# Kernel tuning notes

Measured on AMD Instinct MI355X. Metric: run time of the kernel, lower is better.

The kernel has to match this reference:

```python
import math
import jax, jax.numpy as jnp
import numpy as np

DIM = 128
NUM_PROJ = 256
ENC = jnp.asarray(2 ** np.arange(8), dtype=jnp.uint8)  # [1,2,4,...,128]
DEQUANT_SCALE = math.sqrt(math.pi / 2) / NUM_PROJ


def quantize_packed(x, S):
    # x: (..., dim) float32 -> packed uint8 (..., ceil(num_proj/8))
    projected = jnp.einsum('...d,pd->...p', x, S)
    signs = projected > 0  # bool (..., num_proj)
    pad_len = (-NUM_PROJ) % 8
    if pad_len > 0:
        pad = [(0, 0)] * (signs.ndim - 1) + [(0, pad_len)]
        signs = jnp.pad(signs, pad, constant_values=False)
    signs = signs.reshape(*signs.shape[:-1], -1, 8)  # (..., nbytes, 8)
    packed = jnp.sum(signs.astype(jnp.uint8) * ENC, axis=-1, dtype=jnp.uint8)
    return packed


def unpack_signs(packed):
    # packed: uint8 (..., nbytes) -> {-1,+1} float32 (..., num_proj)
    bits = jnp.bitwise_and(packed[..., None], ENC) > 0  # (..., nbytes, 8)
    bits = bits.reshape(*packed.shape[:-1], -1)[..., :NUM_PROJ]
    return bits.astype(jnp.float32) * 2.0 - 1.0


def setup_inputs() -> dict:
    key = jax.random.key(0)
    k1, k2, k3 = jax.random.split(key, 3)
    query = jax.random.normal(k1, (2, 32, 4096, DIM), dtype=jnp.float32)
    key_t = jax.random.normal(k2, (2, 32, 4096, DIM), dtype=jnp.float32)
    S = jax.random.normal(k3, (NUM_PROJ, DIM), dtype=jnp.float32)
    return {"query": query, "key": key_t, "S": S}


def reference(query, key, S):
    # quantize keys to bit-packed sign sketch, then estimate <query, key>
    packed = quantize_packed(key, S)                       # uint8 (..., 32)
    signs = unpack_signs(packed)                           # (..., 256)
    q_proj = jnp.einsum('...d,pd->...p', query, S)         # (..., 256)
    est = DEQUANT_SCALE * jnp.sum(q_proj * signs, axis=-1) # (B,H,S)
    return est
```

## Files before the change

kernel.cpp:

```cpp
#include <hip/hip_runtime.h>
#include <stdint.h>

#define DIM 128
#define NPROJ 256
#define TPB 128
#define TAU 0.016f
#define QCAP 512
#define DEQ 0.004895758348888673f

typedef _Float16 f16x8 __attribute__((ext_vector_type(8)));
typedef float f32x4 __attribute__((ext_vector_type(4)));

__global__ __launch_bounds__(256) void qjl_prep(const float* __restrict__ Sg,
                                                _Float16* __restrict__ ws) {
    int t = blockIdx.x * 256 + threadIdx.x;
    int lane = t & 63, fid = t >> 6;
    int f = fid & 1, ks = (fid >> 1) & 3, c = fid >> 3;
    int p = c * 32 + f * 16 + (lane & 15);
    int d0 = ks * 32 + (lane >> 4) * 8;
    const float4* s4 = (const float4*)(Sg + p * DIM + d0);
    float4 a = s4[0], b = s4[1];
    f16x8 h = {(_Float16)a.x, (_Float16)a.y, (_Float16)a.z, (_Float16)a.w,
               (_Float16)b.x, (_Float16)b.y, (_Float16)b.z, (_Float16)b.w};
    *(f16x8*)(ws + (size_t)fid * 512 + lane * 8) = h;
}

#define LOADT(buf, C, T)                                                             \
    { _Pragma("unroll")                                                              \
      for (int ks = 0; ks < 4; ++ks)                                                 \
          buf[ks] = *(const f16x8*)(bs + ((C) * 8 + ks * 2 + (T)) * 512 + lane * 8); }

#define LOADA(dst, src)                                                              \
    { const float* rp = (src) + (tok0 + wv * 16 + m) * DIM;                          \
      _Pragma("unroll")                                                              \
      for (int ks = 0; ks < 4; ++ks) {                                               \
          int d0 = ks * 32 + quad * 8;                                               \
          float4 x = *(const float4*)(rp + d0);                                      \
          float4 y = *(const float4*)(rp + d0 + 4);                                  \
          dst[ks] = (f16x8){(_Float16)x.x, (_Float16)x.y, (_Float16)x.z, (_Float16)x.w, \
                            (_Float16)y.x, (_Float16)y.y, (_Float16)y.z, (_Float16)y.w}; } }

#define F_STEP(C, T, buf)                                                            \
    { f32x4 k0 = {0,0,0,0}, q0 = {0,0,0,0};                                          \
      _Pragma("unroll")                                                              \
      for (int ks = 0; ks < 4; ++ks) {                                               \
          k0 = __builtin_amdgcn_mfma_f32_16x16x32_f16(ak[ks], buf[ks], k0, 0,0,0);   \
          q0 = __builtin_amdgcn_mfma_f32_16x16x32_f16(aq[ks], buf[ks], q0, 0,0,0);   \
      }                                                                              \
      _Pragma("unroll")                                                              \
      for (int r = 0; r < 4; ++r) {                                                  \
          uint32_t s0 = __float_as_uint(k0[r]) & 0x80000000u;                        \
          est[r] += __uint_as_float(__float_as_uint(q0[r]) ^ s0);                    \
          if (__builtin_expect(fabsf(k0[r]) < TAU, 0)) {                             \
              int idx = atomicAdd(&qn, 1);                                           \
              if (idx < QCAP) {                                                      \
                  qmeta[idx] = (uint32_t)(wv * 16 + quad * 4 + r)                    \
                      | ((uint32_t)((C) * 32 + (T) * 16 + m) << 8)                   \
                      | ((s0 ? 0u : 1u) << 16);                                      \
                  qval[idx] = q0[r];                                                 \
              }                                                                      \
          } } }

__global__ __launch_bounds__(512, 2) void qjl_main(
    const float* __restrict__ qg, const float* __restrict__ kg,
    const float* __restrict__ Sg, const _Float16* __restrict__ ws,
    float* __restrict__ out)
{
    __shared__ _Float16 bs[32768];
    __shared__ float    est_s[TPB];
    __shared__ uint32_t qmeta[QCAP];
    __shared__ float    qval[QCAP];
    __shared__ int      qn;

    const int tid = threadIdx.x, lane = tid & 63, wv = tid >> 6;
    const int m = lane & 15, quad = lane >> 4;
    const long tok0 = (long)blockIdx.x * TPB;
    if (tid == 0) qn = 0;

    {
        const char* gsrc = (const char*)ws + tid * 16;
        char* ldst = (char*)bs + tid * 16;
        #pragma unroll
        for (int r = 0; r < 8; ++r)
            __builtin_amdgcn_global_load_lds(
                (const __attribute__((address_space(1))) void*)(gsrc + r * 8192),
                (__attribute__((address_space(3))) void*)(ldst + r * 8192),
                16, 0, 0);
    }

    f16x8 ak[4], aq[4];
    f16x8 tA[4], tB[4];
    float est[4] = {0.f, 0.f, 0.f, 0.f};

    LOADA(ak, kg);
    LOADA(aq, qg);
    __syncthreads();

    LOADT(tA, 0, 0);
    LOADT(tB, 0, 1);
    F_STEP(0, 0, tA); LOADT(tA, 1, 0);
    F_STEP(0, 1, tB); LOADT(tB, 1, 1);
    F_STEP(1, 0, tA); LOADT(tA, 2, 0);
    F_STEP(1, 1, tB); LOADT(tB, 2, 1);
    F_STEP(2, 0, tA); LOADT(tA, 3, 0);
    F_STEP(2, 1, tB); LOADT(tB, 3, 1);
    F_STEP(3, 0, tA); LOADT(tA, 4, 0);
    F_STEP(3, 1, tB); LOADT(tB, 4, 1);
    F_STEP(4, 0, tA); LOADT(tA, 5, 0);
    F_STEP(4, 1, tB); LOADT(tB, 5, 1);
    F_STEP(5, 0, tA); LOADT(tA, 6, 0);
    F_STEP(5, 1, tB); LOADT(tB, 6, 1);
    F_STEP(6, 0, tA); LOADT(tA, 7, 0);
    F_STEP(6, 1, tB); LOADT(tB, 7, 1);
    F_STEP(7, 0, tA);
    F_STEP(7, 1, tB);

    #pragma unroll
    for (int r = 0; r < 4; ++r) {
        float e = est[r];
        e += __shfl_xor(e, 1);
        e += __shfl_xor(e, 2);
        e += __shfl_xor(e, 4);
        e += __shfl_xor(e, 8);
        if (m == 0) est_s[wv * 16 + quad * 4 + r] = DEQ * e;
    }
    __syncthreads();

    int nc = qn < QCAP ? qn : QCAP;
    for (int i = tid; i < nc; i += 512) {
        uint32_t mm = qmeta[i];
        int tl = mm & 255;
        int p  = (mm >> 8) & 255;
        int sf = (mm >> 16) & 1;
        const float4* kr = (const float4*)(kg + (tok0 + tl) * DIM);
        const float4* sr = (const float4*)(Sg + (long)p * DIM);
        double dk = 0.0;
        #pragma unroll 8
        for (int j = 0; j < 32; ++j) {
            float4 kv4 = kr[j], sv4 = sr[j];
            dk += (double)kv4.x * (double)sv4.x + (double)kv4.y * (double)sv4.y
                + (double)kv4.z * (double)sv4.z + (double)kv4.w * (double)sv4.w;
        }
        int st = (dk > 0.0) ? 1 : 0;
        if (st != sf) {
            float sg = sf ? 1.f : -1.f;
            atomicAdd(&est_s[tl], -2.f * DEQ * qval[i] * sg);
        }
    }
    __syncthreads();

    if (tid < TPB) out[tok0 + tid] = est_s[tid];
}

extern "C" void kernel_launch(void* const* d_in, const int* in_sizes, int n_in,
                              void* d_out, int out_size, void* d_ws, size_t ws_size,
                              hipStream_t stream) {
    const float* q = (const float*)d_in[0];
    const float* k = (const float*)d_in[1];
    const float* S = (const float*)d_in[2];
    float* out = (float*)d_out;
    _Float16* ws = (_Float16*)d_ws;
    hipLaunchKernelGGL(qjl_prep, dim3(16), dim3(256), 0, stream, S, ws);
    int nblocks = out_size / TPB;
    hipLaunchKernelGGL(qjl_main, dim3(nblocks), dim3(512), 0, stream, q, k, S, ws, out);
}
```

Before: 328.6 us.

## Halve tokens per block and stream projection tiles through a double-buffered LDS

After: 318.3 us. -3.1%, faster.

```diff
diff --git a/kernel.cpp b/kernel.cpp
--- a/kernel.cpp
+++ b/kernel.cpp
@@ -3,7 +3,7 @@
 
 #define DIM 128
 #define NPROJ 256
-#define TPB 128
+#define TPB 64
 #define TAU 0.016f
 #define QCAP 512
 #define DEQ 0.004895758348888673f
@@ -25,10 +25,20 @@
     *(f16x8*)(ws + (size_t)fid * 512 + lane * 8) = h;
 }
 
-#define LOADT(buf, C, T)                                                             \
+#define STAGE(buf, C0)                                                               \
+    { const char* gsrc = (const char*)(ws + (size_t)(C0) * 4096) + tid * 16;         \
+      char* ldst = (char*)(buf) + tid * 16;                                          \
+      _Pragma("unroll")                                                              \
+      for (int r = 0; r < 4; ++r)                                                    \
+          __builtin_amdgcn_global_load_lds(                                          \
+              (const __attribute__((address_space(1))) void*)(gsrc + r * 4096),      \
+              (__attribute__((address_space(3))) void*)(ldst + r * 4096),            \
+              16, 0, 0); }
+
+#define LOADT(dst, buf, CL, T)                                                       \
     { _Pragma("unroll")                                                              \
       for (int ks = 0; ks < 4; ++ks)                                                 \
-          buf[ks] = *(const f16x8*)(bs + ((C) * 8 + ks * 2 + (T)) * 512 + lane * 8); }
+          dst[ks] = *(const f16x8*)((buf) + ((CL) * 8 + ks * 2 + (T)) * 512 + lane * 8); }
 
 #define LOADA(dst, src)                                                              \
     { const float* rp = (src) + (tok0 + wv * 16 + m) * DIM;                          \
@@ -61,12 +71,20 @@
               }                                                                      \
           } } }
 
-__global__ __launch_bounds__(512, 2) void qjl_main(
+#define PHASE(buf, C0)                                                               \
+    LOADT(tA, buf, 0, 0);                                                            \
+    LOADT(tB, buf, 0, 1);                                                            \
+    F_STEP(C0,     0, tA); LOADT(tA, buf, 1, 0);                                     \
+    F_STEP(C0,     1, tB); LOADT(tB, buf, 1, 1);                                     \
+    F_STEP(C0 + 1, 0, tA);                                                           \
+    F_STEP(C0 + 1, 1, tB);
+
+__global__ __launch_bounds__(256, 2) void qjl_main(
     const float* __restrict__ qg, const float* __restrict__ kg,
     const float* __restrict__ Sg, const _Float16* __restrict__ ws,
     float* __restrict__ out)
 {
-    __shared__ _Float16 bs[32768];
+    __shared__ _Float16 bs[2][8192];
     __shared__ float    est_s[TPB];
     __shared__ uint32_t qmeta[QCAP];
     __shared__ float    qval[QCAP];
@@ -77,43 +95,25 @@
     const long tok0 = (long)blockIdx.x * TPB;
     if (tid == 0) qn = 0;
 
-    {
-        const char* gsrc = (const char*)ws + tid * 16;
-        char* ldst = (char*)bs + tid * 16;
-        #pragma unroll
-        for (int r = 0; r < 8; ++r)
-            __builtin_amdgcn_global_load_lds(
-                (const __attribute__((address_space(1))) void*)(gsrc + r * 8192),
-                (__attribute__((address_space(3))) void*)(ldst + r * 8192),
-                16, 0, 0);
-    }
-
     f16x8 ak[4], aq[4];
     f16x8 tA[4], tB[4];
     float est[4] = {0.f, 0.f, 0.f, 0.f};
 
+    STAGE(bs[0], 0);
+    STAGE(bs[1], 2);
     LOADA(ak, kg);
     LOADA(aq, qg);
     __syncthreads();
 
-    LOADT(tA, 0, 0);
-    LOADT(tB, 0, 1);
-    F_STEP(0, 0, tA); LOADT(tA, 1, 0);
-    F_STEP(0, 1, tB); LOADT(tB, 1, 1);
-    F_STEP(1, 0, tA); LOADT(tA, 2, 0);
-    F_STEP(1, 1, tB); LOADT(tB, 2, 1);
-    F_STEP(2, 0, tA); LOADT(tA, 3, 0);
-    F_STEP(2, 1, tB); LOADT(tB, 3, 1);
-    F_STEP(3, 0, tA); LOADT(tA, 4, 0);
-    F_STEP(3, 1, tB); LOADT(tB, 4, 1);
-    F_STEP(4, 0, tA); LOADT(tA, 5, 0);
-    F_STEP(4, 1, tB); LOADT(tB, 5, 1);
-    F_STEP(5, 0, tA); LOADT(tA, 6, 0);
-    F_STEP(5, 1, tB); LOADT(tB, 6, 1);
-    F_STEP(6, 0, tA); LOADT(tA, 7, 0);
-    F_STEP(6, 1, tB); LOADT(tB, 7, 1);
-    F_STEP(7, 0, tA);
-    F_STEP(7, 1, tB);
+    PHASE(bs[0], 0);
+    __syncthreads();
+    STAGE(bs[0], 4);
+    PHASE(bs[1], 2);
+    __syncthreads();
+    STAGE(bs[1], 6);
+    PHASE(bs[0], 4);
+    __syncthreads();
+    PHASE(bs[1], 6);
 
     #pragma unroll
     for (int r = 0; r < 4; ++r) {
@@ -127,7 +127,7 @@
     __syncthreads();
 
     int nc = qn < QCAP ? qn : QCAP;
-    for (int i = tid; i < nc; i += 512) {
+    for (int i = tid; i < nc; i += 256) {
         uint32_t mm = qmeta[i];
         int tl = mm & 255;
         int p  = (mm >> 8) & 255;
@@ -162,5 +162,5 @@
     _Float16* ws = (_Float16*)d_ws;
     hipLaunchKernelGGL(qjl_prep, dim3(16), dim3(256), 0, stream, S, ws);
     int nblocks = out_size / TPB;
-    hipLaunchKernelGGL(qjl_main, dim3(nblocks), dim3(512), 0, stream, q, k, S, ws, out);
+    hipLaunchKernelGGL(qjl_main, dim3(nblocks), dim3(256), 0, stream, q, k, S, ws, out);
 }
```
